# Optimization experiments

Hardware: AMD Instinct MI355X
Metric: run time of the kernel (lower is better)

## Reference

```python
import jax, jax.numpy as jnp
import numpy as np

N, H = 8192, 1024

def setup_inputs() -> dict:
    key = jax.random.key(0)
    ks = jax.random.split(key, 7)
    s = 1.0 / np.sqrt(H)
    return {
        "input_tensor": jax.random.normal(ks[0], (N, H), dtype=jnp.float32),
        "Wq": jax.random.uniform(ks[1], (H, H), dtype=jnp.float32, minval=-s, maxval=s),
        "bq": jax.random.uniform(ks[2], (H,), dtype=jnp.float32, minval=-s, maxval=s),
        "Wk": jax.random.uniform(ks[3], (H, H), dtype=jnp.float32, minval=-s, maxval=s),
        "bk": jax.random.uniform(ks[4], (H,), dtype=jnp.float32, minval=-s, maxval=s),
        "Wv": jax.random.uniform(ks[5], (H, H), dtype=jnp.float32, minval=-s, maxval=s),
        "bv": jax.random.uniform(ks[6], (H,), dtype=jnp.float32, minval=-s, maxval=s),
    }

def reference(input_tensor, Wq, bq, Wk, bk, Wv, bv):
    # torch nn.Linear: x @ W.T + b
    q = input_tensor @ Wq.T + bq  # [N, H]
    k = input_tensor @ Wk.T + bk  # [N, H]
    v = input_tensor @ Wv.T + bv  # [N, H]
    scale = jnp.sqrt(jnp.asarray(input_tensor.shape[1], dtype=q.dtype))
    # (q @ k.T / sqrt(H)) @ v  -- no softmax; same math as original
    scores = (q @ k.T) / scale  # [N, N]
    return scores @ v  # [N, H]
```

## Files before the change

kernel.cpp:

```cpp
#include <hip/hip_runtime.h>
#include <hip/hip_bf16.h>
#include <stdint.h>
#include <stddef.h>

typedef __bf16 bf16_t;
typedef __bf16 bf16x4 __attribute__((ext_vector_type(4)));
typedef __bf16 bf16x8 __attribute__((ext_vector_type(8)));
typedef float  floatx4 __attribute__((ext_vector_type(4)));

#define TK 32

__global__ void prep_w(const float* __restrict__ Wk, bf16_t* __restrict__ Wkb,
                       bf16_t* __restrict__ WkTb,
                       const float* __restrict__ Wv, bf16_t* __restrict__ Wvb,
                       const float* __restrict__ Wq, bf16_t* __restrict__ WqTb,
                       float* __restrict__ svec) {
    __shared__ bf16_t tile[64][72];
    const int b = blockIdx.x;
    const int t = threadIdx.x;
    if (b == 1536) {
        *(float4*)(svec + t * 4) = float4{0.f, 0.f, 0.f, 0.f};
        return;
    }
    if (b >= 512) {
        const int base = (b - 512) * 1024 + t * 4;
        float4 f = *(const float4*)(Wv + base);
        bf16x4 o;
        o.x = (bf16_t)f.x; o.y = (bf16_t)f.y;
        o.z = (bf16_t)f.z; o.w = (bf16_t)f.w;
        *(bf16x4*)(Wvb + base) = o;
        return;
    }
    const bool isK = (b < 256);
    const int bb = b & 255;
    const float* src = isK ? Wk : Wq;
    bf16_t* dT = isK ? WkTb : WqTb;
    const int r0 = (bb >> 4) * 64, c0 = (bb & 15) * 64;
    const int c4 = t & 15;
    const int rbase = t >> 4;
    #pragma unroll
    for (int p = 0; p < 4; ++p) {
        const int r = rbase + 16 * p;
        const size_t gidx = (size_t)(r0 + r) * 1024 + c0 + c4 * 4;
        float4 f = *(const float4*)(src + gidx);
        bf16x4 o;
        o.x = (bf16_t)f.x; o.y = (bf16_t)f.y;
        o.z = (bf16_t)f.z; o.w = (bf16_t)f.w;
        if (isK) *(bf16x4*)(Wkb + gidx) = o;
        *(bf16x4*)&tile[r][c4 * 4] = o;
    }
    __syncthreads();
    #pragma unroll
    for (int p = 0; p < 2; ++p) {
        const int q = t + 256 * p;
        const int cc = q >> 3;
        const int r8 = (q & 7) * 8;
        bf16x8 v;
        #pragma unroll
        for (int u = 0; u < 8; ++u) v[u] = tile[r8 + u][cc];
        *(bf16x8*)(dT + (size_t)(c0 + cc) * 1024 + r0 + r8) = v;
    }
}

__global__ void prep_x_fused(const float* __restrict__ x,
                             bf16_t* __restrict__ xb, bf16_t* __restrict__ xbT,
                             float* __restrict__ svec,
                             const bf16_t* __restrict__ WqTb,
                             const bf16_t* __restrict__ WkTb,
                             bf16_t* __restrict__ W2Tb,
                             const float* __restrict__ bq,
                             float* __restrict__ q1, int SEQ, int H) {
    __shared__ __align__(16) char smem[9472];
    const int L = blockIdx.x;
    const int t = threadIdx.x;
    if (L < 256) {
        bf16_t* As = (bf16_t*)smem;
        bf16_t* Bs = (bf16_t*)(smem + 4096);
        const int bm = (L >> 4) * 64, bn = (L & 15) * 64;
        const int lane = t & 63, wave = t >> 6;
        const int wm = wave >> 1, wn = wave & 1;
        floatx4 acc[2][2] = {};
        const int fr = lane & 15, fk = (lane >> 4) * 8;
        const int sr = t >> 2, so = (t & 3) * 8;
        for (int kt = 0; kt < 1024; kt += TK) {
            __builtin_amdgcn_global_load_lds(
                (const __attribute__((address_space(1))) void*)
                    (WqTb + (size_t)(bm + sr) * 1024 + kt + so),
                (__attribute__((address_space(3))) void*)&As[t * 8], 16, 0, 0);
            __builtin_amdgcn_global_load_lds(
                (const __attribute__((address_space(1))) void*)
                    (WkTb + (size_t)(bn + sr) * 1024 + kt + so),
                (__attribute__((address_space(3))) void*)&Bs[t * 8], 16, 0, 0);
            __syncthreads();
            bf16x8 af[2], bg[2];
            #pragma unroll
            for (int i = 0; i < 2; ++i)
                af[i] = *(const bf16x8*)&As[(wm * 32 + i * 16 + fr) * TK + fk];
            #pragma unroll
            for (int j = 0; j < 2; ++j)
                bg[j] = *(const bf16x8*)&Bs[(wn * 32 + j * 16 + fr) * TK + fk];
            #pragma unroll
            for (int i = 0; i < 2; ++i)
                #pragma unroll
                for (int j = 0; j < 2; ++j)
                    acc[i][j] = __builtin_amdgcn_mfma_f32_16x16x32_bf16(
                        af[i], bg[j], acc[i][j], 0, 0, 0);
            __syncthreads();
        }
        const int rq = (lane >> 4) * 4;
        #pragma unroll
        for (int i = 0; i < 2; ++i)
            #pragma unroll
            for (int j = 0; j < 2; ++j) {
                const int col = bn + wn * 32 + j * 16 + fr;
                #pragma unroll
                for (int r = 0; r < 4; ++r) {
                    const int row = bm + wm * 32 + i * 16 + rq + r;
                    W2Tb[(size_t)row * 1024 + col] = (bf16_t)acc[i][j][r];
                }
            }
        return;
    }
    if (L < 512) {
        const int lane = t & 63, wv = t >> 6;
        const int row = (L - 256) * 4 + wv;
        const bf16_t* mp = WkTb + (size_t)row * 1024;
        float acc = 0.f;
        for (int a = lane * 8; a < 1024; a += 512) {
            bf16x8 m8 = *(const bf16x8*)(mp + a);
            #pragma unroll
            for (int u = 0; u < 8; ++u) acc += (float)m8[u] * bq[a + u];
        }
        #pragma unroll
        for (int off = 32; off; off >>= 1) acc += __shfl_down(acc, off);
        if (lane == 0) q1[row] = acc;
        return;
    }
    bf16_t (*tile)[72] = (bf16_t(*)[72])smem;
    float* csum = (float*)(smem + 9216);
    const int LL = L - 512;
    const int n0 = (LL >> 4) * 64, k0 = (LL & 15) * 64;
    const int c4 = t & 15;
    const int rbase = t >> 4;
    float a0 = 0.f, a1 = 0.f, a2 = 0.f, a3 = 0.f;
    if (t < 64) csum[t] = 0.f;
    #pragma unroll
    for (int p = 0; p < 4; ++p) {
        const int r = rbase + 16 * p;
        const size_t gidx = (size_t)(n0 + r) * H + k0 + c4 * 4;
        float4 f = *(const float4*)(x + gidx);
        bf16x4 o;
        o.x = (bf16_t)f.x; o.y = (bf16_t)f.y;
        o.z = (bf16_t)f.z; o.w = (bf16_t)f.w;
        *(bf16x4*)(xb + gidx) = o;
        *(bf16x4*)&tile[r][c4 * 4] = o;
        a0 += f.x; a1 += f.y; a2 += f.z; a3 += f.w;
    }
    __syncthreads();
    atomicAdd(&csum[c4 * 4 + 0], a0);
    atomicAdd(&csum[c4 * 4 + 1], a1);
    atomicAdd(&csum[c4 * 4 + 2], a2);
    atomicAdd(&csum[c4 * 4 + 3], a3);
    #pragma unroll
    for (int p = 0; p < 2; ++p) {
        const int q = t + 256 * p;
        const int kk = q >> 3;
        const int n8 = (q & 7) * 8;
        bf16x8 v;
        #pragma unroll
        for (int u = 0; u < 8; ++u) v[u] = tile[n8 + u][kk];
        *(bf16x8*)(xbT + (size_t)(k0 + kk) * SEQ + n0 + n8) = v;
    }
    __syncthreads();
    if (t < 64) atomicAdd(svec + k0 + t, csum[t]);
}

__global__ void reduce_bf16(const bf16_t* __restrict__ part,
                            bf16_t* __restrict__ dst, int n, int nsplit,
                            float scale) {
    int i = (blockIdx.x * blockDim.x + threadIdx.x) * 8;
    if (i < n) {
        float acc[8] = {};
        for (int z = 0; z < nsplit; ++z) {
            bf16x8 p = *(const bf16x8*)(part + (size_t)z * n + i);
            #pragma unroll
            for (int u = 0; u < 8; ++u) acc[u] += (float)p[u];
        }
        bf16x8 o;
        #pragma unroll
        for (int u = 0; u < 8; ++u) o[u] = (bf16_t)(acc[u] * scale);
        *(bf16x8*)(dst + i) = o;
    }
}

template <int TMp, int TNp, int MODE, int SWZ, int MERGE, typename OutT>
__global__ __launch_bounds__(256, 2) void gemm_bt(
    const bf16_t* __restrict__ A, const bf16_t* __restrict__ B,
    OutT* __restrict__ C, const float* __restrict__ p1,
    int M, int N, int K, int kChunk, float scale, int ngemm,
    const float* __restrict__ e_bv, const float* __restrict__ e_kv1,
    const float* __restrict__ e_wvs, const float* __restrict__ e_bk, float cN,
    const bf16_t* __restrict__ mvM0, const bf16_t* __restrict__ mvM1,
    const float* __restrict__ mvv, const float* __restrict__ mvv2,
    const float* __restrict__ mvv3, const float* __restrict__ mvv4,
    float* __restrict__ mvy0, float* __restrict__ mvy1, float mvScale)
{
    const int tid = threadIdx.x;
    const int L = blockIdx.x;

    if (MERGE && L >= ngemm) {
        const int lane = tid & 63, wv = tid >> 6;
        if (MERGE == 1) {
            #pragma unroll
            for (int rr = 0; rr < 2; ++rr) {
                const int row = (L - ngemm) * 8 + wv * 2 + rr;
                const bf16_t* mp;
                float* y;
                if (row >= 1024) { mp = mvM1 + (size_t)(row - 1024) * 1024; y = mvy1 + row - 1024; }
                else             { mp = mvM0 + (size_t)row * 1024;          y = mvy0 + row; }
                float acc = 0.f;
                for (int a = lane * 8; a < 1024; a += 512) {
                    bf16x8 m8 = *(const bf16x8*)(mp + a);
                    #pragma unroll
                    for (int u = 0; u < 8; ++u) acc += (float)m8[u] * mvv[a + u];
                }
                #pragma unroll
                for (int off = 32; off; off >>= 1) acc += __shfl_down(acc, off);
                if (lane == 0) *y = acc * mvScale;
            }
        } else if (MERGE == 3) {
            const int row = (L - ngemm) * 4 + wv;
            const bf16_t* mp = mvM0 + (size_t)row * 1024;
            float s1 = 0.f, s2 = 0.f;
            for (int a = lane * 8; a < 1024; a += 512) {
                bf16x8 m8 = *(const bf16x8*)(mp + a);
                #pragma unroll
                for (int u = 0; u < 8; ++u) {
                    const float m = (float)m8[u];
                    s1 += m * mvv[a + u];
                    s2 += m * mvv2[a + u];
                }
            }
            #pragma unroll
            for (int off = 32; off; off >>= 1) {
                s1 += __shfl_down(s1, off);
                s2 += __shfl_down(s2, off);
            }
            if (lane == 0) { mvy0[row] = s1; mvy1[row] = s2; }
        } else {
            const int row = (L - ngemm) * 4 + wv;
            const bf16_t* mp = mvM0 + (size_t)row * 1024;
            float s0 = 0.f, c1 = 0.f, c2 = 0.f;
            for (int a = lane * 8; a < 1024; a += 512) {
                bf16x8 m8 = *(const bf16x8*)(mp + a);
                #pragma unroll
                for (int u = 0; u < 8; ++u) {
                    s0 += (float)m8[u] * mvv[a + u];
                    c1 += mvv3[a + u] * mvv2[a + u];
                    c2 += mvv4[a + u] * mvv2[a + u];
                }
            }
            #pragma unroll
            for (int off = 32; off; off >>= 1) {
                s0 += __shfl_down(s0, off);
                c1 += __shfl_down(c1, off);
                c2 += __shfl_down(c2, off);
            }
            if (lane == 0)
                mvy0[row] = (s0 + e_bv[row] * c1 + (e_wvs[row] + cN * e_bv[row]) * c2) * mvScale;
        }
        return;
    }

    __shared__ __align__(16) bf16_t As[TMp * TK];
    __shared__ __align__(16) bf16_t Bs[TNp * TK];
    constexpr int MF = TMp / 32;
    constexpr int NF = TNp / 32;
    constexpr int nA = TMp / 64;
    constexpr int nB = TNp / 64;

    const int lane = tid & 63;
    const int wave = tid >> 6;
    const int wm   = wave >> 1;
    const int wn   = wave & 1;

    int bm, bn, z;
    if (SWZ == 1) {
        z = ((L & 7) << 1) | (L >> 9);
        const int mn = (L >> 3) & 63;
        bm = (mn >> 3) * TMp; bn = (mn & 7) * TNp;
    } else if (SWZ == 2) {
        bm = ((L & 7) * 8 + ((L >> 3) & 7)) * TMp;
        bn = (L >> 6) * TNp;
        z = 0;
    } else {
        bm = (L >> 4) * TMp;
        bn = (L & 15) * TNp;
        z = 0;
    }
    const int k0 = z * kChunk;
    C += (size_t)z * M * N;

    floatx4 acc[MF][NF] = {};
    const int fr = lane & 15;
    const int fk = (lane >> 4) * 8;

    for (int kt = k0; kt < k0 + kChunk; kt += TK) {
        #pragma unroll
        for (int p = 0; p < nA; ++p) {
            const int c = tid + 256 * p;
            const int r = c >> 2, o = (c & 3) * 8;
            __builtin_amdgcn_global_load_lds(
                (const __attribute__((address_space(1))) void*)
                    (A + (size_t)(bm + r) * K + kt + o),
                (__attribute__((address_space(3))) void*)&As[c * 8], 16, 0, 0);
        }
        #pragma unroll
        for (int p = 0; p < nB; ++p) {
            const int c = tid + 256 * p;
            const int r = c >> 2, o = (c & 3) * 8;
            __builtin_amdgcn_global_load_lds(
                (const __attribute__((address_space(1))) void*)
                    (B + (size_t)(bn + r) * K + kt + o),
                (__attribute__((address_space(3))) void*)&Bs[c * 8], 16, 0, 0);
        }
        __syncthreads();

        bf16x8 af[MF], bg[NF];
        #pragma unroll
        for (int i = 0; i < MF; ++i)
            af[i] = *(const bf16x8*)&As[(wm * (TMp / 2) + i * 16 + fr) * TK + fk];
        #pragma unroll
        for (int j = 0; j < NF; ++j)
            bg[j] = *(const bf16x8*)&Bs[(wn * (TNp / 2) + j * 16 + fr) * TK + fk];
        #pragma unroll
        for (int i = 0; i < MF; ++i) {
            #pragma unroll
            for (int j = 0; j < NF; ++j) {
                acc[i][j] = __builtin_amdgcn_mfma_f32_16x16x32_bf16(
                    af[i], bg[j], acc[i][j], 0, 0, 0);
            }
        }
        __syncthreads();
    }

    const int rq = (lane >> 4) * 4;
    #pragma unroll
    for (int i = 0; i < MF; ++i) {
        #pragma unroll
        for (int j = 0; j < NF; ++j) {
            const int col = bn + wn * (TNp / 2) + j * 16 + fr;
            #pragma unroll
            for (int r = 0; r < 4; ++r) {
                const int row = bm + wm * (TMp / 2) + i * 16 + rq + r;
                float v = acc[i][j][r];
                if (MODE == 3)
                    v += e_bv[row] * e_kv1[col] + (e_wvs[row] + cN * e_bv[row]) * e_bk[col];
                v *= scale;
                if (MODE == 1) v += p1[col];
                C[(size_t)row * N + col] = (OutT)v;
            }
        }
    }
}

extern "C" void kernel_launch(void* const* d_in, const int* in_sizes, int n_in,
                              void* d_out, int out_size, void* d_ws, size_t ws_size,
                              hipStream_t stream) {
    const int SEQ = 8192;
    const int H   = 1024;

    const float* x  = (const float*)d_in[0];
    const float* Wq = (const float*)d_in[1];
    const float* bq = (const float*)d_in[2];
    const float* Wk = (const float*)d_in[3];
    const float* bk = (const float*)d_in[4];
    const float* Wv = (const float*)d_in[5];
    const float* bv = (const float*)d_in[6];
    float* out = (float*)d_out;

    const size_t MI = 1024 * 1024;
    char* ws = (char*)d_ws;
    bf16_t* xb   = (bf16_t*)(ws);
    bf16_t* xbT  = (bf16_t*)(ws + 16 * MI);
    bf16_t* Wkb  = (bf16_t*)(ws + 32 * MI);
    bf16_t* Wvb  = (bf16_t*)(ws + 34 * MI);
    bf16_t* WqTb = (bf16_t*)(ws + 36 * MI);
    bf16_t* Gb   = (bf16_t*)(ws + 38 * MI);
    bf16_t* S1b  = (bf16_t*)(ws + 40 * MI);
    bf16_t* W2Tb = (bf16_t*)(ws + 42 * MI);
    bf16_t* Utb  = (bf16_t*)(ws + 44 * MI);
    float*  svec = (float*)(ws + 46 * MI);
    float*  kv1  = svec + 1024;
    float*  wvs  = svec + 2048;
    float*  cvec = svec + 3072;
    float*  q1   = svec + 4096;
    float*  r1   = svec + 5120;
    float*  r2   = svec + 6144;
    bf16_t* part = (bf16_t*)(ws + 48 * MI);
    bf16_t* WkTb = (bf16_t*)(ws + 80 * MI);

    dim3 blk(256);
    const float inv32 = 1.0f / 32.0f;
    const int nHH = H * H;
    const int rgrid = nHH / 8 / 256;
    const float* nf = nullptr;
    const bf16_t* nb = nullptr;
    float* nfm = nullptr;

    prep_w<<<dim3(1537), blk, 0, stream>>>(Wk, Wkb, WkTb, Wv, Wvb, Wq, WqTb, svec);
    prep_x_fused<<<dim3(2560), blk, 0, stream>>>(
        x, xb, xbT, svec, WqTb, WkTb, W2Tb, bq, q1, SEQ, H);
    gemm_bt<128, 128, 0, 1, 1, bf16_t><<<dim3(1280), blk, 0, stream>>>(
        xbT, xbT, part, nf, H, H, SEQ, SEQ / 16, 1.0f, 1024,
        nf, nf, nf, nf, 0.f, Wkb, Wvb, svec, nf, nf, nf, kv1, wvs, 1.0f);
    reduce_bf16<<<dim3(rgrid), blk, 0, stream>>>(part, Gb, nHH, 16, 1.0f);
    gemm_bt<64, 64, 0, 4, 3, bf16_t><<<dim3(512), blk, 0, stream>>>(
        Wvb, Gb, S1b, nf, H, H, H, H, 1.0f, 256,
        nf, nf, nf, nf, 0.f, WqTb, nb, kv1, bk, nf, nf, r1, r2, 1.0f);
    gemm_bt<64, 64, 3, 4, 4, bf16_t><<<dim3(512), blk, 0, stream>>>(
        S1b, W2Tb, Utb, nf, H, H, H, H, inv32, 256,
        bv, r1, wvs, r2, (float)SEQ, S1b, nb, q1, bq, kv1, bk, cvec, nfm, inv32);
    gemm_bt<128, 128, 1, 2, 0, float><<<dim3(512), blk, 0, stream>>>(
        xb, Utb, out, cvec, SEQ, H, H, H, 1.0f, 1 << 30,
        nf, nf, nf, nf, 0.f, nb, nb, nf, nf, nf, nf, nfm, nfm, 0.f);
}
```

Measured before the change: 199.7 us.

## Exploit symmetry of Gram matrix X^T X to compute only upper-triangular tiles

Result: faster. 195.3 us (-2.2%).

```diff
diff --git a/kernel.cpp b/kernel.cpp
--- a/kernel.cpp
+++ b/kernel.cpp
@@ -175,22 +175,39 @@
     if (t < 64) atomicAdd(svec + k0 + t, csum[t]);
 }
 
-__global__ void reduce_bf16(const bf16_t* __restrict__ part,
-                            bf16_t* __restrict__ dst, int n, int nsplit,
-                            float scale) {
-    int i = (blockIdx.x * blockDim.x + threadIdx.x) * 8;
-    if (i < n) {
-        float acc[8] = {};
-        for (int z = 0; z < nsplit; ++z) {
-            bf16x8 p = *(const bf16x8*)(part + (size_t)z * n + i);
-            #pragma unroll
-            for (int u = 0; u < 8; ++u) acc[u] += (float)p[u];
-        }
-        bf16x8 o;
-        #pragma unroll
-        for (int u = 0; u < 8; ++u) o[u] = (bf16_t)(acc[u] * scale);
-        *(bf16x8*)(dst + i) = o;
-    }
+__global__ void reduce_sym(const bf16_t* __restrict__ part,
+                           bf16_t* __restrict__ dst) {
+    __shared__ bf16_t lds[16][128];
+    const int t = threadIdx.x;
+    int t36 = blockIdx.x >> 3;
+    const int chunk = blockIdx.x & 7;
+    int i = 0;
+    while (t36 >= 8 - i) { t36 -= 8 - i; ++i; }
+    const int j = i + t36;
+    const int r0 = chunk * 16;
+    const int rr = t >> 4;
+    const int c8 = (t & 15) * 8;
+    const int row = i * 128 + r0 + rr;
+    const size_t off = (size_t)row * 1024 + j * 128 + c8;
+    float a8[8] = {};
+    for (int z = 0; z < 16; ++z) {
+        bf16x8 p = *(const bf16x8*)(part + (size_t)z * 1024 * 1024 + off);
+        #pragma unroll
+        for (int u = 0; u < 8; ++u) a8[u] += (float)p[u];
+    }
+    bf16x8 o;
+    #pragma unroll
+    for (int u = 0; u < 8; ++u) o[u] = (bf16_t)a8[u];
+    *(bf16x8*)(dst + off) = o;
+    if (i == j) return;
+    *(bf16x8*)&lds[rr][c8] = o;
+    __syncthreads();
+    const int c = t >> 1;
+    const int half = t & 1;
+    bf16x8 v;
+    #pragma unroll
+    for (int u = 0; u < 8; ++u) v[u] = lds[half * 8 + u][c];
+    *(bf16x8*)(dst + (size_t)(j * 128 + c) * 1024 + i * 128 + r0 + half * 8) = v;
 }
 
 template <int TMp, int TNp, int MODE, int SWZ, int MERGE, typename OutT>
@@ -285,14 +302,17 @@
     const int wn   = wave & 1;
 
     int bm, bn, z;
-    if (SWZ == 1) {
-        z = ((L & 7) << 1) | (L >> 9);
-        const int mn = (L >> 3) & 63;
-        bm = (mn >> 3) * TMp; bn = (mn & 7) * TNp;
-    } else if (SWZ == 2) {
+    if (SWZ == 2) {
         bm = ((L & 7) * 8 + ((L >> 3) & 7)) * TMp;
         bn = (L >> 6) * TNp;
         z = 0;
+    } else if (SWZ == 5) {
+        z = ((L & 7) << 1) | (L >= 288 ? 1 : 0);
+        int t36 = (L >> 3) % 36;
+        int ti = 0;
+        while (t36 >= 8 - ti) { t36 -= 8 - ti; ++ti; }
+        bm = ti * TMp;
+        bn = (ti + t36) * TNp;
     } else {
         bm = (L >> 4) * TMp;
         bn = (L & 15) * TNp;
@@ -402,8 +422,6 @@
 
     dim3 blk(256);
     const float inv32 = 1.0f / 32.0f;
-    const int nHH = H * H;
-    const int rgrid = nHH / 8 / 256;
     const float* nf = nullptr;
     const bf16_t* nb = nullptr;
     float* nfm = nullptr;
@@ -411,10 +429,10 @@
     prep_w<<<dim3(1537), blk, 0, stream>>>(Wk, Wkb, WkTb, Wv, Wvb, Wq, WqTb, svec);
     prep_x_fused<<<dim3(2560), blk, 0, stream>>>(
         x, xb, xbT, svec, WqTb, WkTb, W2Tb, bq, q1, SEQ, H);
-    gemm_bt<128, 128, 0, 1, 1, bf16_t><<<dim3(1280), blk, 0, stream>>>(
-        xbT, xbT, part, nf, H, H, SEQ, SEQ / 16, 1.0f, 1024,
+    gemm_bt<128, 128, 0, 5, 1, bf16_t><<<dim3(832), blk, 0, stream>>>(
+        xbT, xbT, part, nf, H, H, SEQ, SEQ / 16, 1.0f, 576,
         nf, nf, nf, nf, 0.f, Wkb, Wvb, svec, nf, nf, nf, kv1, wvs, 1.0f);
-    reduce_bf16<<<dim3(rgrid), blk, 0, stream>>>(part, Gb, nHH, 16, 1.0f);
+    reduce_sym<<<dim3(288), blk, 0, stream>>>(part, Gb);
     gemm_bt<64, 64, 0, 4, 3, bf16_t><<<dim3(512), blk, 0, stream>>>(
         Wvb, Gb, S1b, nf, H, H, H, H, 1.0f, 256,
         nf, nf, nf, nf, 0.f, WqTb, nb, kv1, bk, nf, nf, r1, r2, 1.0f);
```
